# Performance work log

Measured on AMD Instinct MI355X. Metric: run time of the kernel, lower is better.

## Reference

```python
import jax, jax.numpy as jnp
import numpy as np
import math

D = 1024
N_HEAD = 16
HEAD_D = D // N_HEAD

def setup_inputs() -> dict:
    key = jax.random.key(0)
    ks = jax.random.split(key, 10)
    b, s = 4, 2048
    scale = 1.0 / math.sqrt(D)
    inp = {
        "decoder_hs": jax.random.normal(ks[0], (b, s, D), dtype=jnp.float32),
        "encoder_hs": jax.random.normal(ks[1], (b, s, D), dtype=jnp.float32),
        "Wq": jax.random.normal(ks[2], (D, D), dtype=jnp.float32) * scale,
        "bq": jnp.zeros((D,), dtype=jnp.float32),
        "Wk": jax.random.normal(ks[3], (D, D), dtype=jnp.float32) * scale,
        "bk": jnp.zeros((D,), dtype=jnp.float32),
        "Wv": jax.random.normal(ks[4], (D, D), dtype=jnp.float32) * scale,
        "bv": jnp.zeros((D,), dtype=jnp.float32),
        "Wp": jax.random.normal(ks[5], (D, D), dtype=jnp.float32) * scale,
        "bp": jnp.zeros((D,), dtype=jnp.float32),
    }
    return inp

def _split_heads(x, b, s):
    # [b, s, d] -> [b, n_head, s, head_d]
    return x.reshape(b, s, N_HEAD, HEAD_D).transpose(0, 2, 1, 3)

def reference(decoder_hs, encoder_hs, Wq, bq, Wk, bk, Wv, bv, Wp, bp):
    b, s, d = decoder_hs.shape
    # torch nn.Linear: y = x @ W.T + b
    q = _split_heads(decoder_hs @ Wq.T + bq, b, s)
    k = _split_heads(encoder_hs @ Wk.T + bk, b, s)
    v = _split_heads(encoder_hs @ Wv.T + bv, b, s)
    att = jnp.einsum('bhqd,bhkd->bhqk', q, k) * (1.0 / math.sqrt(HEAD_D))
    att = jax.nn.softmax(att, axis=-1)  # mask is None, dropout = 0 (eval)
    y = jnp.einsum('bhqk,bhkd->bhqd', att, v)
    y = y.transpose(0, 2, 1, 3).reshape(b, s, d)
    return y @ Wp.T + bp
```

## Files before the change

### kernel.cpp

```cpp
#include <hip/hip_runtime.h>
#include <hip/hip_bf16.h>

typedef __attribute__((ext_vector_type(8))) short bf16x8;
typedef __attribute__((ext_vector_type(4))) float floatx4;
typedef __attribute__((ext_vector_type(16))) float floatx16;
typedef __attribute__((ext_vector_type(2))) int int2v;

#define MFMA_16x16x32(A, B, C) __builtin_amdgcn_mfma_f32_16x16x32_bf16(A, B, C, 0, 0, 0)
#define MFMA_32x32x16(A, B, C) __builtin_amdgcn_mfma_f32_32x32x16_bf16(A, B, C, 0, 0, 0)

__device__ __forceinline__ unsigned short f2b(float f) {
    __hip_bfloat16 h = __float2bfloat16(f);
    unsigned short u;
    __builtin_memcpy(&u, &h, 2);
    return u;
}
__device__ __forceinline__ unsigned pk2(float a, float b) {
    __hip_bfloat162 h = __float22bfloat162_rn(float2{a, b});
    unsigned u;
    __builtin_memcpy(&u, &h, 4);
    return u;
}
__device__ __forceinline__ bf16x8 mk8(int a, int b, int c, int d) {
    union { int u[4]; bf16x8 v; } x;
    x.u[0] = a; x.u[1] = b; x.u[2] = c; x.u[3] = d;
    return x.v;
}
__device__ __forceinline__ void async_lds16(const void* g, void* l) {
    __builtin_amdgcn_global_load_lds((__attribute__((address_space(1))) void*)g,
                                     (__attribute__((address_space(3))) void*)l, 16, 0, 0);
}

struct CvtArgs {
    const float* src[6];
    unsigned short* dst[6];
    float scale[6];
    int n8[6];
};
__global__ __launch_bounds__(256) void convert_kernel(CvtArgs a) {
    const int t = blockIdx.y;
    const int i = blockIdx.x * 256 + threadIdx.x;
    if (i >= a.n8[t]) return;
    const float sc = a.scale[t];
    const float4* s = (const float4*)a.src[t];
    const float4 x = s[2 * i], y = s[2 * i + 1];
    bf16x8 v;
    v[0] = (short)f2b(x.x * sc); v[1] = (short)f2b(x.y * sc);
    v[2] = (short)f2b(x.z * sc); v[3] = (short)f2b(x.w * sc);
    v[4] = (short)f2b(y.x * sc); v[5] = (short)f2b(y.y * sc);
    v[6] = (short)f2b(y.z * sc); v[7] = (short)f2b(y.w * sc);
    *(bf16x8*)(a.dst[t] + (size_t)i * 8) = v;
}

struct QKVArgs {
    const unsigned short* A[3];
    const unsigned short* B[3];
    const float* bias[3];
    float bscale[3];
    unsigned short* C[3];
};
__global__ __launch_bounds__(256) void gemm_qkv(QKVArgs args) {
    constexpr int M = 8192, N = 1024, K = 1024;
    __shared__ __align__(16) unsigned short As[2][4096];
    __shared__ __align__(16) unsigned short Bs[2][4096];

    const int z = blockIdx.z;
    const unsigned short* __restrict__ A = args.A[z];
    const unsigned short* __restrict__ B = args.B[z];
    const float* __restrict__ bias = args.bias[z];
    const float bsc = args.bscale[z];
    unsigned short* __restrict__ C = args.C[z];

    const int tid  = threadIdx.x;
    const int wave = tid >> 6;
    const int lane = tid & 63;
    const int l16  = lane & 15;
    const int quad = lane >> 4;
    const int bm = (blockIdx.x & 63) * 128;
    const int bn = (blockIdx.x >> 6) * 128;
    const int wm = (wave >> 1) * 64;
    const int wn = (wave & 1) * 64;

    const int srow = tid >> 2;
    const int skb  = (tid & 3) * 8;

    floatx4 acc[4][4] = {};

    auto stage = [&](int buf, int k0) {
        async_lds16(A + (size_t)(bm + srow) * K + skb + k0, &As[buf][tid * 8]);
        async_lds16(A + (size_t)(bm + 64 + srow) * K + skb + k0, &As[buf][2048 + tid * 8]);
        async_lds16(B + (size_t)(bn + srow) * K + skb + k0, &Bs[buf][tid * 8]);
        async_lds16(B + (size_t)(bn + 64 + srow) * K + skb + k0, &Bs[buf][2048 + tid * 8]);
    };

    stage(0, 0);
    for (int it = 0; it < K / 32; ++it) {
        __syncthreads();
        if (it + 1 < K / 32) stage((it + 1) & 1, (it + 1) * 32);
        const unsigned short* Ac = &As[it & 1][0];
        const unsigned short* Bc = &Bs[it & 1][0];

        bf16x8 af[4], bfr[4];
        #pragma unroll
        for (int i = 0; i < 4; ++i)
            af[i] = *(const bf16x8*)&Ac[(wm + i * 16 + l16) * 32 + quad * 8];
        #pragma unroll
        for (int j = 0; j < 4; ++j)
            bfr[j] = *(const bf16x8*)&Bc[(wn + j * 16 + l16) * 32 + quad * 8];
        #pragma unroll
        for (int i = 0; i < 4; ++i)
            #pragma unroll
            for (int j = 0; j < 4; ++j)
                acc[i][j] = MFMA_16x16x32(af[i], bfr[j], acc[i][j]);
    }

    if (z == 2) {
        __syncthreads();
        unsigned short* Tw = &As[0][0] + wave * (16 * 66);
        #pragma unroll
        for (int j = 0; j < 4; ++j) {
            const float bv = bias[bn + wn + j * 16 + l16] * bsc;
            #pragma unroll
            for (int i = 0; i < 4; ++i)
                #pragma unroll
                for (int r = 0; r < 4; ++r)
                    Tw[l16 * 66 + i * 16 + quad * 4 + r] = f2b(acc[i][j][r] + bv);
            __syncthreads();
            const int c2  = lane >> 2;
            const int tch = lane & 3;
            bf16x8 t0 = *(const bf16x8*)&Tw[c2 * 66 + tch * 16];
            bf16x8 t1 = *(const bf16x8*)&Tw[c2 * 66 + tch * 16 + 8];
            const size_t off = (size_t)(bn + wn + j * 16 + c2) * (size_t)M + (bm + wm + tch * 16);
            *(bf16x8*)&C[off]     = t0;
            *(bf16x8*)&C[off + 8] = t1;
            __syncthreads();
        }
    } else {
        #pragma unroll
        for (int i = 0; i < 4; ++i) {
            const int row = bm + wm + i * 16 + quad * 4;
            #pragma unroll
            for (int j = 0; j < 4; ++j) {
                const int col = bn + wn + j * 16 + l16;
                const float bv = bias[col] * bsc;
                #pragma unroll
                for (int r = 0; r < 4; ++r)
                    C[(size_t)(row + r) * N + col] = f2b(acc[i][j][r] + bv);
            }
        }
    }
}

__global__ __launch_bounds__(256) void gemm_out(
    const unsigned short* __restrict__ A, const unsigned short* __restrict__ B,
    const float* __restrict__ bias, float* __restrict__ C,
    int M, int N, int K)
{
    __shared__ __align__(16) unsigned short As[2][4096];
    __shared__ __align__(16) unsigned short Bs[2][4096];

    const int tid  = threadIdx.x;
    const int wave = tid >> 6;
    const int lane = tid & 63;
    const int l16  = lane & 15;
    const int quad = lane >> 4;
    const int bm = (blockIdx.x & 63) * 128;
    const int bn = (blockIdx.x >> 6) * 128;
    const int wm = (wave >> 1) * 64;
    const int wn = (wave & 1) * 64;

    const int srow = tid >> 2;
    const int skb  = (tid & 3) * 8;

    floatx4 acc[4][4] = {};

    auto stage = [&](int buf, int k0) {
        async_lds16(A + (size_t)(bm + srow) * K + skb + k0, &As[buf][tid * 8]);
        async_lds16(A + (size_t)(bm + 64 + srow) * K + skb + k0, &As[buf][2048 + tid * 8]);
        async_lds16(B + (size_t)(bn + srow) * K + skb + k0, &Bs[buf][tid * 8]);
        async_lds16(B + (size_t)(bn + 64 + srow) * K + skb + k0, &Bs[buf][2048 + tid * 8]);
    };

    stage(0, 0);
    for (int it = 0; it < K / 32; ++it) {
        __syncthreads();
        if (it + 1 < K / 32) stage((it + 1) & 1, (it + 1) * 32);
        const unsigned short* Ac = &As[it & 1][0];
        const unsigned short* Bc = &Bs[it & 1][0];

        bf16x8 af[4], bfr[4];
        #pragma unroll
        for (int i = 0; i < 4; ++i)
            af[i] = *(const bf16x8*)&Ac[(wm + i * 16 + l16) * 32 + quad * 8];
        #pragma unroll
        for (int j = 0; j < 4; ++j)
            bfr[j] = *(const bf16x8*)&Bc[(wn + j * 16 + l16) * 32 + quad * 8];
        #pragma unroll
        for (int i = 0; i < 4; ++i)
            #pragma unroll
            for (int j = 0; j < 4; ++j)
                acc[i][j] = MFMA_16x16x32(af[i], bfr[j], acc[i][j]);
    }

    #pragma unroll
    for (int i = 0; i < 4; ++i) {
        const int row = bm + wm + i * 16 + quad * 4;
        #pragma unroll
        for (int j = 0; j < 4; ++j) {
            const int col = bn + wn + j * 16 + l16;
            const float bv = bias[col];
            #pragma unroll
            for (int r = 0; r < 4; ++r)
                C[(size_t)(row + r) * N + col] = acc[i][j][r] + bv;
        }
    }
}

__global__ __launch_bounds__(256, 4) void attn_kernel(
    const unsigned short* __restrict__ Q, const unsigned short* __restrict__ Kg,
    const unsigned short* __restrict__ Vt, unsigned short* __restrict__ Y)
{
    __shared__ __align__(16) unsigned short Ks[2][4096];
    __shared__ __align__(16) unsigned short Vs[2][4096];
    __shared__ float rsb[4][32];

    const int tid  = threadIdx.x;
    const int wave = tid >> 6;
    const int lane = tid & 63;
    const int l31  = lane & 31;
    const int hi   = lane >> 5;
    const int x7   = lane & 7;
    const int bh = blockIdx.x & 63;
    const int qt = blockIdx.x >> 6;
    const int b  = bh >> 4;
    const int h  = bh & 15;
    const int q0 = qt * 128 + wave * 32;
    const size_t base  = ((size_t)b * 2048) * 1024 + (size_t)h * 64;
    const size_t vbase = ((size_t)h * 64) * 8192 + (size_t)b * 2048;

    bf16x8 qf[4];
    {
        const size_t qrow = base + (size_t)(q0 + l31) * 1024 + hi * 8;
        #pragma unroll
        for (int ks = 0; ks < 4; ++ks)
            qf[ks] = *(const bf16x8*)&Q[qrow + ks * 16];
    }

    const floatx16 Z16 = {0.f,0.f,0.f,0.f,0.f,0.f,0.f,0.f,
                          0.f,0.f,0.f,0.f,0.f,0.f,0.f,0.f};

    floatx16 o0 = Z16, o1 = Z16;
    float racc = 0.f;

    const int r0  = tid >> 3;
    const int csw = (tid & 7) ^ (r0 & 7);

    int co[4];
    #pragma unroll
    for (int ks = 0; ks < 4; ++ks) co[ks] = (((ks * 2 + hi) ^ x7) * 8);
    const int krow = l31 * 64;

    auto stage = [&](int buf, int kv0) {
        async_lds16(&Kg[base + (size_t)(kv0 + r0) * 1024 + csw * 8],      &Ks[buf][tid * 8]);
        async_lds16(&Kg[base + (size_t)(kv0 + 32 + r0) * 1024 + csw * 8], &Ks[buf][2048 + tid * 8]);
        async_lds16(&Vt[vbase + (size_t)r0 * 8192 + kv0 + csw * 8],        &Vs[buf][tid * 8]);
        async_lds16(&Vt[vbase + (size_t)(r0 + 32) * 8192 + kv0 + csw * 8], &Vs[buf][2048 + tid * 8]);
    };

    auto procP = [&](const floatx16& st, bf16x8& paA, bf16x8& paB) {
        float e[16];
        #pragma unroll
        for (int i = 0; i < 16; ++i) e[i] = __builtin_amdgcn_exp2f(st[i]);
        racc += ((e[0]+e[1])+(e[2]+e[3])) + ((e[4]+e[5])+(e[6]+e[7]))
              + ((e[8]+e[9])+(e[10]+e[11])) + ((e[12]+e[13])+(e[14]+e[15]));
        const int w0 = (int)pk2(e[0],  e[1]);
        const int w1 = (int)pk2(e[2],  e[3]);
        const int w2 = (int)pk2(e[4],  e[5]);
        const int w3 = (int)pk2(e[6],  e[7]);
        const int w4 = (int)pk2(e[8],  e[9]);
        const int w5 = (int)pk2(e[10], e[11]);
        const int w6 = (int)pk2(e[12], e[13]);
        const int w7 = (int)pk2(e[14], e[15]);
        const int2v a0 = __builtin_amdgcn_permlane32_swap(w0, w2, false, false);
        const int2v a1 = __builtin_amdgcn_permlane32_swap(w1, w3, false, false);
        const int2v a2 = __builtin_amdgcn_permlane32_swap(w4, w6, false, false);
        const int2v a3 = __builtin_amdgcn_permlane32_swap(w5, w7, false, false);
        paA = mk8(a0.x, a1.x, a0.y, a1.y);
        paB = mk8(a2.x, a3.x, a2.y, a3.y);
    };

    stage(0, 0);
    for (int t = 0; t < 32; ++t) {
        __syncthreads();
        if (t < 31) stage((t + 1) & 1, (t + 1) * 64);
        const unsigned short* Kc = &Ks[t & 1][0];
        const unsigned short* Vc = &Vs[t & 1][0];

        floatx16 st0 = Z16, st1 = Z16;
        __builtin_amdgcn_s_setprio(1);
        #pragma unroll
        for (int ks = 0; ks < 4; ++ks) {
            const bf16x8 kf0 = *(const bf16x8*)&Kc[krow + co[ks]];
            const bf16x8 kf1 = *(const bf16x8*)&Kc[2048 + krow + co[ks]];
            st0 = MFMA_32x32x16(kf0, qf[ks], st0);
            st1 = MFMA_32x32x16(kf1, qf[ks], st1);
        }
        __builtin_amdgcn_s_setprio(0);

        bf16x8 pa[4];
        procP(st0, pa[0], pa[1]);
        procP(st1, pa[2], pa[3]);

        __builtin_amdgcn_s_setprio(1);
        #pragma unroll
        for (int f = 0; f < 4; ++f) {
            const bf16x8 v0 = *(const bf16x8*)&Vc[krow + co[f]];
            const bf16x8 v1 = *(const bf16x8*)&Vc[2048 + krow + co[f]];
            o0 = MFMA_32x32x16(pa[f], v0, o0);
            o1 = MFMA_32x32x16(pa[f], v1, o1);
        }
        __builtin_amdgcn_s_setprio(0);
    }

    const int ri = __float_as_int(racc);
    const int2v rsw = __builtin_amdgcn_permlane32_swap(ri, ri, false, false);
    const float total = __int_as_float(rsw.x) + __int_as_float(rsw.y);
    rsb[wave][l31] = total;
    #pragma unroll
    for (int g = 0; g < 4; ++g) {
        const floatx4 rq = *(const floatx4*)&rsb[wave][4 * hi + 8 * g];
        #pragma unroll
        for (int e2 = 0; e2 < 4; ++e2) {
            const float inv = 1.0f / rq[e2];
            const int reg = g * 4 + e2;
            const size_t row = q0 + 8 * g + 4 * hi + e2;
            Y[base + row * 1024 + l31]      = f2b(o0[reg] * inv);
            Y[base + row * 1024 + 32 + l31] = f2b(o1[reg] * inv);
        }
    }
}

extern "C" void kernel_launch(void* const* d_in, const int* in_sizes, int n_in,
                              void* d_out, int out_size, void* d_ws, size_t ws_size,
                              hipStream_t stream)
{
    const float* dec = (const float*)d_in[0];
    const float* enc = (const float*)d_in[1];
    const float* Wq  = (const float*)d_in[2];
    const float* bq  = (const float*)d_in[3];
    const float* Wk  = (const float*)d_in[4];
    const float* bk  = (const float*)d_in[5];
    const float* Wv  = (const float*)d_in[6];
    const float* bv  = (const float*)d_in[7];
    const float* Wp  = (const float*)d_in[8];
    const float* bp  = (const float*)d_in[9];

    const size_t NTOK = 8192, DM = 1024;
    unsigned short* ws = (unsigned short*)d_ws;
    unsigned short* decB = ws;
    unsigned short* encB = decB + NTOK * DM;
    unsigned short* WqB  = encB + NTOK * DM;
    unsigned short* WkB  = WqB + DM * DM;
    unsigned short* WvB  = WkB + DM * DM;
    unsigned short* WpB  = WvB + DM * DM;
    unsigned short* Qb   = WpB + DM * DM;
    unsigned short* Kb   = Qb + NTOK * DM;
    unsigned short* VtG  = Kb + NTOK * DM;
    unsigned short* Yb   = VtG + NTOK * DM;

    const float C_SM = 0.18033688f;

    CvtArgs a;
    a.src[0] = dec; a.src[1] = enc; a.src[2] = Wq; a.src[3] = Wk; a.src[4] = Wv; a.src[5] = Wp;
    a.dst[0] = decB; a.dst[1] = encB; a.dst[2] = WqB; a.dst[3] = WkB; a.dst[4] = WvB; a.dst[5] = WpB;
    a.scale[0] = 1.f; a.scale[1] = 1.f; a.scale[2] = C_SM;
    a.scale[3] = 1.f; a.scale[4] = 1.f; a.scale[5] = 1.f;
    a.n8[0] = a.n8[1] = (int)(NTOK * DM / 8);
    a.n8[2] = a.n8[3] = a.n8[4] = a.n8[5] = (int)(DM * DM / 8);
    convert_kernel<<<dim3(4096, 6), 256, 0, stream>>>(a);

    QKVArgs qa;
    qa.A[0] = decB; qa.A[1] = encB; qa.A[2] = encB;
    qa.B[0] = WqB;  qa.B[1] = WkB;  qa.B[2] = WvB;
    qa.bias[0] = bq; qa.bias[1] = bk; qa.bias[2] = bv;
    qa.bscale[0] = C_SM; qa.bscale[1] = 1.f; qa.bscale[2] = 1.f;
    qa.C[0] = Qb;   qa.C[1] = Kb;   qa.C[2] = VtG;
    gemm_qkv<<<dim3(512, 1, 3), 256, 0, stream>>>(qa);

    attn_kernel<<<dim3(1024), 256, 0, stream>>>(Qb, Kb, VtG, Yb);
    gemm_out<<<dim3(512), 256, 0, stream>>>(Yb, WpB, bp, (float*)d_out, 8192, 1024, 1024);
}
```

Baseline: 324.8 us.

## Enlarge GEMM tiles to 256x128, swizzle LDS, compute softmax row sums via MFMA

The QKV and output GEMMs move to 512-thread blocks computing 256x128 tiles, so each B tile is reused across twice as many rows, and an XOR swizzle is applied to the LDS k-chunk layout to cut bank conflicts. The attention kernel drops the scalar exp-sum, permlane swap and LDS reduction, and instead accumulates row sums with an extra MFMA against a ones vector. It also adjusts its K/V LDS swizzle. This adds one MFMA per P·V step and raises per-block register and LDS pressure in exchange for better reuse and fewer conflicts.

New measurement: 323.6 us. About the same (-0.3%).

```diff
diff --git a/kernel.cpp b/kernel.cpp
--- a/kernel.cpp
+++ b/kernel.cpp
@@ -59,9 +59,9 @@
     float bscale[3];
     unsigned short* C[3];
 };
-__global__ __launch_bounds__(256) void gemm_qkv(QKVArgs args) {
+__global__ __launch_bounds__(512, 2) void gemm_qkv(QKVArgs args) {
     constexpr int M = 8192, N = 1024, K = 1024;
-    __shared__ __align__(16) unsigned short As[2][4096];
+    __shared__ __align__(16) unsigned short As[2][8192];
     __shared__ __align__(16) unsigned short Bs[2][4096];
 
     const int z = blockIdx.z;
@@ -76,21 +76,21 @@
     const int lane = tid & 63;
     const int l16  = lane & 15;
     const int quad = lane >> 4;
-    const int bm = (blockIdx.x & 63) * 128;
-    const int bn = (blockIdx.x >> 6) * 128;
+    const int bm = (blockIdx.x & 31) * 256;
+    const int bn = (blockIdx.x >> 5) * 128;
     const int wm = (wave >> 1) * 64;
     const int wn = (wave & 1) * 64;
 
     const int srow = tid >> 2;
-    const int skb  = (tid & 3) * 8;
+    const int skb  = (((tid & 3) ^ ((tid >> 2) & 3) ^ ((tid >> 4) & 3)) * 8);
+    const int cq   = ((quad ^ (l16 & 3) ^ ((l16 >> 2) & 3)) * 8);
 
     floatx4 acc[4][4] = {};
 
     auto stage = [&](int buf, int k0) {
-        async_lds16(A + (size_t)(bm + srow) * K + skb + k0, &As[buf][tid * 8]);
-        async_lds16(A + (size_t)(bm + 64 + srow) * K + skb + k0, &As[buf][2048 + tid * 8]);
-        async_lds16(B + (size_t)(bn + srow) * K + skb + k0, &Bs[buf][tid * 8]);
-        async_lds16(B + (size_t)(bn + 64 + srow) * K + skb + k0, &Bs[buf][2048 + tid * 8]);
+        async_lds16(A + (size_t)(bm + srow) * K + skb + k0,       &As[buf][tid * 8]);
+        async_lds16(A + (size_t)(bm + 128 + srow) * K + skb + k0, &As[buf][4096 + tid * 8]);
+        async_lds16(B + (size_t)(bn + srow) * K + skb + k0,       &Bs[buf][tid * 8]);
     };
 
     stage(0, 0);
@@ -103,10 +103,10 @@
         bf16x8 af[4], bfr[4];
         #pragma unroll
         for (int i = 0; i < 4; ++i)
-            af[i] = *(const bf16x8*)&Ac[(wm + i * 16 + l16) * 32 + quad * 8];
+            af[i] = *(const bf16x8*)&Ac[(wm + i * 16 + l16) * 32 + cq];
         #pragma unroll
         for (int j = 0; j < 4; ++j)
-            bfr[j] = *(const bf16x8*)&Bc[(wn + j * 16 + l16) * 32 + quad * 8];
+            bfr[j] = *(const bf16x8*)&Bc[(wn + j * 16 + l16) * 32 + cq];
         #pragma unroll
         for (int i = 0; i < 4; ++i)
             #pragma unroll
@@ -151,12 +151,12 @@
     }
 }
 
-__global__ __launch_bounds__(256) void gemm_out(
+__global__ __launch_bounds__(512, 2) void gemm_out(
     const unsigned short* __restrict__ A, const unsigned short* __restrict__ B,
     const float* __restrict__ bias, float* __restrict__ C,
     int M, int N, int K)
 {
-    __shared__ __align__(16) unsigned short As[2][4096];
+    __shared__ __align__(16) unsigned short As[2][8192];
     __shared__ __align__(16) unsigned short Bs[2][4096];
 
     const int tid  = threadIdx.x;
@@ -164,21 +164,21 @@
     const int lane = tid & 63;
     const int l16  = lane & 15;
     const int quad = lane >> 4;
-    const int bm = (blockIdx.x & 63) * 128;
-    const int bn = (blockIdx.x >> 6) * 128;
+    const int bm = (blockIdx.x & 31) * 256;
+    const int bn = (blockIdx.x >> 5) * 128;
     const int wm = (wave >> 1) * 64;
     const int wn = (wave & 1) * 64;
 
     const int srow = tid >> 2;
-    const int skb  = (tid & 3) * 8;
+    const int skb  = (((tid & 3) ^ ((tid >> 2) & 3) ^ ((tid >> 4) & 3)) * 8);
+    const int cq   = ((quad ^ (l16 & 3) ^ ((l16 >> 2) & 3)) * 8);
 
     floatx4 acc[4][4] = {};
 
     auto stage = [&](int buf, int k0) {
-        async_lds16(A + (size_t)(bm + srow) * K + skb + k0, &As[buf][tid * 8]);
-        async_lds16(A + (size_t)(bm + 64 + srow) * K + skb + k0, &As[buf][2048 + tid * 8]);
-        async_lds16(B + (size_t)(bn + srow) * K + skb + k0, &Bs[buf][tid * 8]);
-        async_lds16(B + (size_t)(bn + 64 + srow) * K + skb + k0, &Bs[buf][2048 + tid * 8]);
+        async_lds16(A + (size_t)(bm + srow) * K + skb + k0,       &As[buf][tid * 8]);
+        async_lds16(A + (size_t)(bm + 128 + srow) * K + skb + k0, &As[buf][4096 + tid * 8]);
+        async_lds16(B + (size_t)(bn + srow) * K + skb + k0,       &Bs[buf][tid * 8]);
     };
 
     stage(0, 0);
@@ -191,10 +191,10 @@
         bf16x8 af[4], bfr[4];
         #pragma unroll
         for (int i = 0; i < 4; ++i)
-            af[i] = *(const bf16x8*)&Ac[(wm + i * 16 + l16) * 32 + quad * 8];
+            af[i] = *(const bf16x8*)&Ac[(wm + i * 16 + l16) * 32 + cq];
         #pragma unroll
         for (int j = 0; j < 4; ++j)
-            bfr[j] = *(const bf16x8*)&Bc[(wn + j * 16 + l16) * 32 + quad * 8];
+            bfr[j] = *(const bf16x8*)&Bc[(wn + j * 16 + l16) * 32 + cq];
         #pragma unroll
         for (int i = 0; i < 4; ++i)
             #pragma unroll
@@ -222,7 +222,6 @@
 {
     __shared__ __align__(16) unsigned short Ks[2][4096];
     __shared__ __align__(16) unsigned short Vs[2][4096];
-    __shared__ float rsb[4][32];
 
     const int tid  = threadIdx.x;
     const int wave = tid >> 6;
@@ -230,6 +229,7 @@
     const int l31  = lane & 31;
     const int hi   = lane >> 5;
     const int x7   = lane & 7;
+    const int h4   = ((lane >> 4) & 1) << 2;
     const int bh = blockIdx.x & 63;
     const int qt = blockIdx.x >> 6;
     const int b  = bh >> 4;
@@ -246,18 +246,21 @@
             qf[ks] = *(const bf16x8*)&Q[qrow + ks * 16];
     }
 
+    bf16x8 ones;
+    #pragma unroll
+    for (int e = 0; e < 8; ++e) ones[e] = (short)0x3F80;
     const floatx16 Z16 = {0.f,0.f,0.f,0.f,0.f,0.f,0.f,0.f,
                           0.f,0.f,0.f,0.f,0.f,0.f,0.f,0.f};
 
     floatx16 o0 = Z16, o1 = Z16;
-    float racc = 0.f;
+    floatx16 rs = Z16;
 
     const int r0  = tid >> 3;
-    const int csw = (tid & 7) ^ (r0 & 7);
+    const int csw = (tid & 7) ^ (r0 & 7) ^ (((tid >> 7) & 1) << 2);
 
     int co[4];
     #pragma unroll
-    for (int ks = 0; ks < 4; ++ks) co[ks] = (((ks * 2 + hi) ^ x7) * 8);
+    for (int ks = 0; ks < 4; ++ks) co[ks] = (((ks * 2 + hi) ^ x7 ^ h4) * 8);
     const int krow = l31 * 64;
 
     auto stage = [&](int buf, int kv0) {
@@ -271,8 +274,6 @@
         float e[16];
         #pragma unroll
         for (int i = 0; i < 16; ++i) e[i] = __builtin_amdgcn_exp2f(st[i]);
-        racc += ((e[0]+e[1])+(e[2]+e[3])) + ((e[4]+e[5])+(e[6]+e[7]))
-              + ((e[8]+e[9])+(e[10]+e[11])) + ((e[12]+e[13])+(e[14]+e[15]));
         const int w0 = (int)pk2(e[0],  e[1]);
         const int w1 = (int)pk2(e[2],  e[3]);
         const int w2 = (int)pk2(e[4],  e[5]);
@@ -318,21 +319,17 @@
             const bf16x8 v1 = *(const bf16x8*)&Vc[2048 + krow + co[f]];
             o0 = MFMA_32x32x16(pa[f], v0, o0);
             o1 = MFMA_32x32x16(pa[f], v1, o1);
+            rs = MFMA_32x32x16(pa[f], ones, rs);
         }
         __builtin_amdgcn_s_setprio(0);
     }
 
-    const int ri = __float_as_int(racc);
-    const int2v rsw = __builtin_amdgcn_permlane32_swap(ri, ri, false, false);
-    const float total = __int_as_float(rsw.x) + __int_as_float(rsw.y);
-    rsb[wave][l31] = total;
     #pragma unroll
     for (int g = 0; g < 4; ++g) {
-        const floatx4 rq = *(const floatx4*)&rsb[wave][4 * hi + 8 * g];
         #pragma unroll
         for (int e2 = 0; e2 < 4; ++e2) {
-            const float inv = 1.0f / rq[e2];
             const int reg = g * 4 + e2;
+            const float inv = 1.0f / rs[reg];
             const size_t row = q0 + 8 * g + 4 * hi + e2;
             Y[base + row * 1024 + l31]      = f2b(o0[reg] * inv);
             Y[base + row * 1024 + 32 + l31] = f2b(o1[reg] * inv);
@@ -385,8 +382,8 @@
     qa.bias[0] = bq; qa.bias[1] = bk; qa.bias[2] = bv;
     qa.bscale[0] = C_SM; qa.bscale[1] = 1.f; qa.bscale[2] = 1.f;
     qa.C[0] = Qb;   qa.C[1] = Kb;   qa.C[2] = VtG;
-    gemm_qkv<<<dim3(512, 1, 3), 256, 0, stream>>>(qa);
+    gemm_qkv<<<dim3(256, 1, 3), 512, 0, stream>>>(qa);
 
     attn_kernel<<<dim3(1024), 256, 0, stream>>>(Qb, Kb, VtG, Yb);
-    gemm_out<<<dim3(512), 256, 0, stream>>>(Yb, WpB, bp, (float*)d_out, 8192, 1024, 1024);
-}
+    gemm_out<<<dim3(256), 512, 0, stream>>>(Yb, WpB, bp, (float*)d_out, 8192, 1024, 1024);
+}
```
